# Kernel tuning notes

Measured on AMD Instinct MI355X. Metric: run time of the kernel, lower is better.

Reference implementation:

```python
import jax, jax.numpy as jnp
import numpy as np

EPS = 0.1

def setup_inputs() -> dict:
    key = jax.random.key(0)
    k1, k2, k3, k4, k5, k6 = jax.random.split(key, 6)
    B, N, Cin, Cout = 8, 2048, 128, 128
    x = jax.random.normal(k1, (B, N, Cin), dtype=jnp.float32)
    x_0 = jax.random.normal(k2, (B, N, Cout), dtype=jnp.float32)
    adj = jax.random.randint(k3, (B, N, N), 0, 2, dtype=jnp.int32)
    # learned parameters (Linear without bias stores weight [out,in]; we keep [in,out])
    W_lin = jax.random.normal(k4, (Cin, Cout), dtype=jnp.float32) / np.sqrt(Cin)
    w_att_l = jax.random.normal(k5, (Cout,), dtype=jnp.float32) / np.sqrt(Cout)
    w_att_r = jax.random.normal(k6, (Cout,), dtype=jnp.float32) / np.sqrt(Cout)
    return {"x": x, "x_0": x_0, "adj": adj, "W_lin": W_lin, "w_att_l": w_att_l, "w_att_r": w_att_r}

def reference(x, x_0, adj, W_lin, w_att_l, w_att_r):
    # x: [B,N,Cin] -> h: [B,N,Cout]
    h = jnp.einsum('bni,io->bno', x, W_lin)
    alpha_l = jnp.einsum('bno,o->bn', h, w_att_l)  # [B,N]
    alpha_r = jnp.einsum('bno,o->bn', h, w_att_r)  # [B,N]
    # alpha[b,i,j] = tanh(alpha_r[b,i] * alpha_l[b,j])
    alpha = jnp.tanh(alpha_r[:, :, None] * alpha_l[:, None, :])  # [B,N,N]
    alpha = jnp.where(adj == 0, jnp.float32(0.0), alpha)
    # dropout p=0.0 -> identity
    out = jnp.einsum('bij,bjo->bio', alpha, h)  # [B,N,Cout]
    return out + EPS * x_0
```

## Files before the change

kernel.cpp:

```cpp
#include <hip/hip_runtime.h>
#include <stdint.h>

#define B_   8
#define N_   2048
#define C_   128
#define EPS_ 0.1f

typedef __attribute__((ext_vector_type(8))) short short8;
typedef __attribute__((ext_vector_type(4))) float f32x4;

__device__ __forceinline__ unsigned short f2bf(float f) {
    union { float f; uint32_t u; } v; v.f = f;
    uint32_t u = v.u + 0x7FFF + ((v.u >> 16) & 1);
    return (unsigned short)(u >> 16);
}

__global__ __launch_bounds__(128) void k_wt(const float* __restrict__ W,
                                            unsigned short* __restrict__ Wt) {
    const int o = blockIdx.x, k = threadIdx.x;
    Wt[o * C_ + k] = f2bf(W[k * C_ + o]);
}

__global__ __launch_bounds__(256) void k_h(
    const float* __restrict__ x, const unsigned short* __restrict__ Wt,
    const float* __restrict__ wl, const float* __restrict__ wr,
    unsigned short* __restrict__ ht, float* __restrict__ al, float* __restrict__ ar)
{
    const int b    = blockIdx.x >> 5;
    const int i0   = (blockIdx.x & 31) * 64;
    const int t    = threadIdx.x;
    const int lane = t & 63;
    const int wid  = t >> 6;

    __shared__ __align__(16) unsigned short xs[64 * 128];
    __shared__ __align__(16) unsigned short ws[128 * 128];

    #pragma unroll
    for (int p = 0; p < 4; ++p) {
        const int s = p * 256 + t, row = s >> 4, u = s & 15;
        const float* gp = x + ((size_t)(b * N_ + i0 + row) * C_ + u * 8);
        float4 f0 = *(const float4*)gp;
        float4 f1 = *(const float4*)(gp + 4);
        short8 tv;
        tv[0] = (short)f2bf(f0.x); tv[1] = (short)f2bf(f0.y);
        tv[2] = (short)f2bf(f0.z); tv[3] = (short)f2bf(f0.w);
        tv[4] = (short)f2bf(f1.x); tv[5] = (short)f2bf(f1.y);
        tv[6] = (short)f2bf(f1.z); tv[7] = (short)f2bf(f1.w);
        *(short8*)&xs[row * 128 + (u ^ (row & 15)) * 8] = tv;
    }
    #pragma unroll
    for (int p = 0; p < 8; ++p) {
        const int s = p * 256 + t, o = s >> 4, u = s & 15;
        int4 v = *(const int4*)(Wt + o * C_ + u * 8);
        *(int4*)&ws[o * 128 + (u ^ (o & 15)) * 8] = v;
    }
    __syncthreads();

    const int m0 = wid * 16, lr = lane & 15, q = lane >> 4;
    f32x4 acc[8];
    #pragma unroll
    for (int i = 0; i < 8; ++i) acc[i] = (f32x4){0.f, 0.f, 0.f, 0.f};

    #pragma unroll
    for (int s = 0; s < 4; ++s) {
        const int m = m0 + lr;
        short8 af = *(const short8*)&xs[m * 128 + ((s * 4 + q) ^ (m & 15)) * 8];
        #pragma unroll
        for (int tt = 0; tt < 8; ++tt) {
            const int o = tt * 16 + lr;
            short8 bf = *(const short8*)&ws[o * 128 + ((s * 4 + q) ^ (o & 15)) * 8];
            acc[tt] = __builtin_amdgcn_mfma_f32_16x16x32_bf16(af, bf, acc[tt], 0, 0, 0);
        }
    }

    float pl[4] = {0.f, 0.f, 0.f, 0.f}, pr[4] = {0.f, 0.f, 0.f, 0.f};
    const int j0 = i0 + m0 + q * 4;
    #pragma unroll
    for (int tt = 0; tt < 8; ++tt) {
        const int o = tt * 16 + lr;
        const float wlv = wl[o], wrv = wr[o];
        unsigned int lo = (unsigned int)f2bf(acc[tt][0]) | ((unsigned int)f2bf(acc[tt][1]) << 16);
        unsigned int hi = (unsigned int)f2bf(acc[tt][2]) | ((unsigned int)f2bf(acc[tt][3]) << 16);
        uint2 u2; u2.x = lo; u2.y = hi;
        *(uint2*)&ht[((size_t)(b * C_ + o)) * N_ + j0] = u2;
        #pragma unroll
        for (int r = 0; r < 4; ++r) {
            pl[r] = fmaf(acc[tt][r], wlv, pl[r]);
            pr[r] = fmaf(acc[tt][r], wrv, pr[r]);
        }
    }
    #pragma unroll
    for (int msk = 1; msk < 16; msk <<= 1) {
        #pragma unroll
        for (int r = 0; r < 4; ++r) {
            pl[r] += __shfl_xor(pl[r], msk, 64);
            pr[r] += __shfl_xor(pr[r], msk, 64);
        }
    }
    if (lr == 0) {
        #pragma unroll
        for (int r = 0; r < 4; ++r) {
            al[b * N_ + j0 + r] = pl[r];
            ar[b * N_ + j0 + r] = pr[r];
        }
    }
}

struct PrefO {
    int4   a0, a1;
    float4 l0, l1;
    int4   h0, h1, h2, h3;
};

__global__ __launch_bounds__(256, 2) void k_out(
    const int* __restrict__ adj, const unsigned short* __restrict__ ht,
    const float* __restrict__ al, const float* __restrict__ ar,
    const float* __restrict__ x0, float* __restrict__ out)
{
    const int b    = blockIdx.x >> 6;
    const int i0   = (blockIdx.x & 63) * 32;
    const int t    = threadIdx.x;
    const int lane = t & 63;
    const int wid  = t >> 6;
    const int m0   = (wid & 1) * 16, n0 = (wid >> 1) * 64;
    const int r    = lane & 15, q = lane >> 4;

    const int row  = i0 + m0 + r;
    const float arv = ar[b * N_ + row];

    const int*            adjp = adj + ((size_t)(b * N_ + row)) * N_ + q * 8;
    const float*          alp  = al + b * N_ + q * 8;
    const unsigned short* hb   = ht + (size_t)b * C_ * N_ + q * 8;
    const unsigned short* hp0  = hb + (size_t)(n0 +  0 + r) * N_;
    const unsigned short* hp1  = hb + (size_t)(n0 + 16 + r) * N_;
    const unsigned short* hp2  = hb + (size_t)(n0 + 32 + r) * N_;
    const unsigned short* hp3  = hb + (size_t)(n0 + 48 + r) * N_;

    auto ld = [&](int s) -> PrefO {
        PrefO P; const int jb = s * 32;
        P.a0 = *(const int4*)(adjp + jb);
        P.a1 = *(const int4*)(adjp + jb + 4);
        P.l0 = *(const float4*)(alp + jb);
        P.l1 = *(const float4*)(alp + jb + 4);
        P.h0 = *(const int4*)(hp0 + jb);
        P.h1 = *(const int4*)(hp1 + jb);
        P.h2 = *(const int4*)(hp2 + jb);
        P.h3 = *(const int4*)(hp3 + jb);
        return P;
    };

    f32x4 acc[4];
    #pragma unroll
    for (int i = 0; i < 4; ++i) acc[i] = (f32x4){0.f, 0.f, 0.f, 0.f};

    auto step = [&](const PrefO& P) {
        const int*   av = (const int*)&P.a0;
        const float* lv = (const float*)&P.l0;
        short8 af;
        #pragma unroll
        for (int e = 0; e < 8; ++e) {
            float z  = arv * lv[e];
            float ex = __expf(2.f * z);
            float th = 1.f - 2.f * __builtin_amdgcn_rcpf(ex + 1.f);
            af[e] = av[e] ? (short)f2bf(th) : (short)0;
        }
        acc[0] = __builtin_amdgcn_mfma_f32_16x16x32_bf16(af, *(const short8*)&P.h0, acc[0], 0, 0, 0);
        acc[1] = __builtin_amdgcn_mfma_f32_16x16x32_bf16(af, *(const short8*)&P.h1, acc[1], 0, 0, 0);
        acc[2] = __builtin_amdgcn_mfma_f32_16x16x32_bf16(af, *(const short8*)&P.h2, acc[2], 0, 0, 0);
        acc[3] = __builtin_amdgcn_mfma_f32_16x16x32_bf16(af, *(const short8*)&P.h3, acc[3], 0, 0, 0);
    };

    PrefO A = ld(0);
    PrefO Bp = ld(1);
    for (int it = 0; it < 32; ++it) {
        step(A);
        if (it < 31) A = ld(2 * it + 2);
        step(Bp);
        if (it < 31) Bp = ld(2 * it + 3);
    }

    #pragma unroll
    for (int tt = 0; tt < 4; ++tt) {
        const int o = n0 + tt * 16 + r;
        #pragma unroll
        for (int rr = 0; rr < 4; ++rr) {
            const int orow = i0 + m0 + q * 4 + rr;
            const size_t idx = ((size_t)(b * N_) + orow) * C_ + o;
            out[idx] = acc[tt][rr] + EPS_ * x0[idx];
        }
    }
}

extern "C" void kernel_launch(void* const* d_in, const int* in_sizes, int n_in,
                              void* d_out, int out_size, void* d_ws, size_t ws_size,
                              hipStream_t stream) {
    const float* x   = (const float*)d_in[0];
    const float* x0  = (const float*)d_in[1];
    const int*   adj = (const int*)d_in[2];
    const float* W   = (const float*)d_in[3];
    const float* wl  = (const float*)d_in[4];
    const float* wr  = (const float*)d_in[5];
    float* out = (float*)d_out;

    unsigned short* ht = (unsigned short*)d_ws;
    float* al = (float*)((char*)d_ws + (size_t)B_ * C_ * N_ * 2);
    float* ar = al + B_ * N_;
    unsigned short* Wt = (unsigned short*)(ar + B_ * N_);

    k_wt <<<C_,             C_,  0, stream>>>(W, Wt);
    k_h  <<<B_ * (N_ / 64), 256, 0, stream>>>(x, Wt, wl, wr, ht, al, ar);
    k_out<<<B_ * (N_ / 32), 256, 0, stream>>>(adj, ht, al, ar, x0, out);
}
```

Before: 283.1 us.

## Pre-pack adjacency into bitmask before attention-aggregation kernel

```diff
diff --git a/kernel.cpp b/kernel.cpp
--- a/kernel.cpp
+++ b/kernel.cpp
@@ -13,6 +13,27 @@
     union { float f; uint32_t u; } v; v.f = f;
     uint32_t u = v.u + 0x7FFF + ((v.u >> 16) & 1);
     return (unsigned short)(u >> 16);
+}
+
+__global__ __launch_bounds__(256) void k_pack(const int* __restrict__ adj,
+                                              unsigned int* __restrict__ pk) {
+    __shared__ unsigned char bytes[256];
+    const int g = blockIdx.x, t = threadIdx.x;
+    const size_t base = ((size_t)g * 256 + t) * 8;
+    int4 a = *(const int4*)(adj + base);
+    int4 b = *(const int4*)(adj + base + 4);
+    unsigned int m =
+        (a.x ? 1u   : 0u) | (a.y ? 2u   : 0u) | (a.z ? 4u  : 0u) | (a.w ? 8u   : 0u) |
+        (b.x ? 16u  : 0u) | (b.y ? 32u  : 0u) | (b.z ? 64u : 0u) | (b.w ? 128u : 0u);
+    bytes[t] = (unsigned char)m;
+    __syncthreads();
+    if (t < 64) {
+        unsigned int w = (unsigned int)bytes[4*t]
+                       | ((unsigned int)bytes[4*t+1] << 8)
+                       | ((unsigned int)bytes[4*t+2] << 16)
+                       | ((unsigned int)bytes[4*t+3] << 24);
+        pk[(size_t)g * 64 + t] = w;
+    }
 }
 
 __global__ __launch_bounds__(128) void k_wt(const float* __restrict__ W,
@@ -107,13 +128,13 @@
 }
 
 struct PrefO {
-    int4   a0, a1;
+    unsigned int w;
     float4 l0, l1;
     int4   h0, h1, h2, h3;
 };
 
 __global__ __launch_bounds__(256, 2) void k_out(
-    const int* __restrict__ adj, const unsigned short* __restrict__ ht,
+    const unsigned int* __restrict__ pk, const unsigned short* __restrict__ ht,
     const float* __restrict__ al, const float* __restrict__ ar,
     const float* __restrict__ x0, float* __restrict__ out)
 {
@@ -125,10 +146,10 @@
     const int m0   = (wid & 1) * 16, n0 = (wid >> 1) * 64;
     const int r    = lane & 15, q = lane >> 4;
 
-    const int row  = i0 + m0 + r;
+    const int row   = i0 + m0 + r;
     const float arv = ar[b * N_ + row];
 
-    const int*            adjp = adj + ((size_t)(b * N_ + row)) * N_ + q * 8;
+    const unsigned int*   pkp  = pk + ((size_t)(b * N_ + row)) * (N_ / 32);
     const float*          alp  = al + b * N_ + q * 8;
     const unsigned short* hb   = ht + (size_t)b * C_ * N_ + q * 8;
     const unsigned short* hp0  = hb + (size_t)(n0 +  0 + r) * N_;
@@ -138,8 +159,7 @@
 
     auto ld = [&](int s) -> PrefO {
         PrefO P; const int jb = s * 32;
-        P.a0 = *(const int4*)(adjp + jb);
-        P.a1 = *(const int4*)(adjp + jb + 4);
+        P.w  = pkp[s];
         P.l0 = *(const float4*)(alp + jb);
         P.l1 = *(const float4*)(alp + jb + 4);
         P.h0 = *(const int4*)(hp0 + jb);
@@ -154,15 +174,15 @@
     for (int i = 0; i < 4; ++i) acc[i] = (f32x4){0.f, 0.f, 0.f, 0.f};
 
     auto step = [&](const PrefO& P) {
-        const int*   av = (const int*)&P.a0;
         const float* lv = (const float*)&P.l0;
+        const unsigned int wbits = P.w >> (q * 8);
         short8 af;
         #pragma unroll
         for (int e = 0; e < 8; ++e) {
             float z  = arv * lv[e];
             float ex = __expf(2.f * z);
             float th = 1.f - 2.f * __builtin_amdgcn_rcpf(ex + 1.f);
-            af[e] = av[e] ? (short)f2bf(th) : (short)0;
+            af[e] = ((wbits >> e) & 1u) ? (short)f2bf(th) : (short)0;
         }
         acc[0] = __builtin_amdgcn_mfma_f32_16x16x32_bf16(af, *(const short8*)&P.h0, acc[0], 0, 0, 0);
         acc[1] = __builtin_amdgcn_mfma_f32_16x16x32_bf16(af, *(const short8*)&P.h1, acc[1], 0, 0, 0);
@@ -170,7 +190,7 @@
         acc[3] = __builtin_amdgcn_mfma_f32_16x16x32_bf16(af, *(const short8*)&P.h3, acc[3], 0, 0, 0);
     };
 
-    PrefO A = ld(0);
+    PrefO A  = ld(0);
     PrefO Bp = ld(1);
     for (int it = 0; it < 32; ++it) {
         step(A);
@@ -206,8 +226,10 @@
     float* al = (float*)((char*)d_ws + (size_t)B_ * C_ * N_ * 2);
     float* ar = al + B_ * N_;
     unsigned short* Wt = (unsigned short*)(ar + B_ * N_);
-
-    k_wt <<<C_,             C_,  0, stream>>>(W, Wt);
-    k_h  <<<B_ * (N_ / 64), 256, 0, stream>>>(x, Wt, wl, wr, ht, al, ar);
-    k_out<<<B_ * (N_ / 32), 256, 0, stream>>>(adj, ht, al, ar, x0, out);
-}
+    unsigned int*   pkb = (unsigned int*)(Wt + C_ * C_);
+
+    k_pack<<<(B_ * N_ * N_) / 2048, 256, 0, stream>>>(adj, pkb);
+    k_wt  <<<C_,             C_,  0, stream>>>(W, Wt);
+    k_h   <<<B_ * (N_ / 64), 256, 0, stream>>>(x, Wt, wl, wr, ht, al, ar);
+    k_out <<<B_ * (N_ / 32), 256, 0, stream>>>(pkb, ht, al, ar, x0, out);
+}
```

Measured after the change: 294.6 us. +4.1%, slower.
